# Optimization experiments

Measured on AMD Instinct MI355X. Metric: run time of the kernel, lower is better.

The kernel has to match this reference:

```python
import jax, jax.numpy as jnp
import numpy as np
from jax import lax

N, D, M, H = 8192, 32, 8, 128
ATOL = 1e-5
RTOL = 1e-5
MAX_STEPS = 10   # bounded adaptive dopri5 iterations (accept/reject with masking)
DT0 = 0.25


def setup_inputs() -> dict:
    key = jax.random.key(0)
    ks = jax.random.split(key, 6)
    p = lambda k, shape, s: jax.random.normal(k, shape, jnp.float32) * s
    return {
        "z": jax.random.normal(ks[0], (N, D), jnp.float32),
        "G_w": p(ks[1], (M, D), 0.3),
        "W1": p(ks[2], (H, D), (1.0 / D) ** 0.5),
        "b1": jnp.zeros((H,), jnp.float32),
        "W2": p(ks[3], (H, H), (1.0 / H) ** 0.5),
        "b2": jnp.zeros((H,), jnp.float32),
        "W3": p(ks[4], (D, H), (1.0 / H) ** 0.5),
        "b3": jnp.zeros((D,), jnp.float32),
        "T": jnp.ones((1,), jnp.float32),
    }


def qpnf_forward(z, G_w, W1, b1, W2, b2, W3, b3, T):
    d = z.shape[1]

    def mlp(x):  # dF network: d -> 128 -> 128 -> d
        h = jax.nn.relu(x @ W1.T + b1)
        h = jax.nn.relu(h @ W2.T + b2)
        return h @ W3.T + b3

    # G is linear (no bias) so jacrev(G)(x) == G_w for every sample; the batched
    # dG @ dG^T solves collapse to one shared (m,m) solve / (d,d) projector.
    A = G_w @ G_w.T                       # (m, m)
    AinvG = jnp.linalg.solve(A, G_w)      # (m, d) = A^{-1} W
    P = G_w.T @ AinvG                     # (d, d) null-space projector W^T A^{-1} W
    IP = jnp.eye(d, dtype=z.dtype) - P
    trP = jnp.trace(P)

    jac_mlp = jax.vmap(jax.jacrev(lambda xi: mlp(xi[None, :])[0]))  # (N,d,d)

    def f(y):  # augmented state y = [x | logp], dlogp/dt = -div(dx/dx)
        x = y[:, :d]
        dF = mlp(x)                        # (N, d)
        g = x @ G_w.T                      # (N, m)
        dz = -(dF @ IP) - g @ AinvG        # -(eta_J) - (eta_C)
        JdF = jac_mlp(x)                   # (N, d, d)
        # J_f = -(I-P) JdF - P  ->  dlogp = -trace(J_f)
        dlogp = jnp.einsum('jk,nkj->n', IP, JdF) + trP
        return jnp.concatenate([dz, dlogp[:, None]], axis=1)

    def rk_step(y, dt):  # Dormand-Prince 5(4)
        k1 = f(y)
        k2 = f(y + dt * (0.2 * k1))
        k3 = f(y + dt * (3/40 * k1 + 9/40 * k2))
        k4 = f(y + dt * (44/45 * k1 - 56/15 * k2 + 32/9 * k3))
        k5 = f(y + dt * (19372/6561 * k1 - 25360/2187 * k2 + 64448/6561 * k3 - 212/729 * k4))
        k6 = f(y + dt * (9017/3168 * k1 - 355/33 * k2 + 46732/5247 * k3 + 49/176 * k4 - 5103/18656 * k5))
        y1 = y + dt * (35/384 * k1 + 500/1113 * k3 + 125/192 * k4 - 2187/6784 * k5 + 11/84 * k6)
        k7 = f(y1)
        err = dt * ((35/384 - 5179/57600) * k1 + (500/1113 - 7571/16695) * k3
                    + (125/192 - 393/640) * k4 + (-2187/6784 + 92097/339200) * k5
                    + (11/84 - 187/2100) * k6 - (1/40) * k7)
        return y1, err

    t1 = 2.0 * T[0]  # eval path: integration_times[-1] *= 2
    y0 = jnp.concatenate([z, jnp.zeros((z.shape[0], 1), z.dtype)], axis=1)

    def body(carry, _):
        t, dt, y = carry
        done = t >= t1 - 1e-9
        dtc = jnp.where(done, jnp.asarray(1e-3, z.dtype), jnp.minimum(dt, t1 - t))
        y1, ev = rk_step(y, dtc)
        tol = ATOL + RTOL * jnp.maximum(jnp.abs(y), jnp.abs(y1))
        errn = jnp.sqrt(jnp.mean((ev / tol) ** 2))
        accept = jnp.logical_and(~done, errn <= 1.0)
        y_new = jnp.where(accept, y1, y)
        t_new = jnp.where(accept, t + dtc, t)
        factor = jnp.clip(0.9 * errn ** (-0.2), 0.2, 10.0)
        dt_new = jnp.where(done, dt, jnp.clip(dtc * factor, 1e-6, t1))
        dt_new = lax.stop_gradient(dt_new)
        return (t_new, dt_new, y_new), None

    init = (jnp.asarray(0.0, z.dtype), jnp.asarray(DT0, z.dtype), y0)
    (_, _, yT), _ = lax.scan(body, init, None, length=MAX_STEPS)
    return yT[:, :d]


def reference(z, G_w, W1, b1, W2, b2, W3, b3, T):
    return qpnf_forward(z, G_w, W1, b1, W2, b2, W3, b3, T)
```

## Files before the change

kernel.cpp:

```cpp
#include <hip/hip_runtime.h>
#include <hip/hip_cooperative_groups.h>
#include <math.h>

namespace cg = cooperative_groups;
typedef float4 f4;

#define NT 512
#define RB 32

#define WS_WR    0
#define WS_PART  32768
#define WS_TOTAL 35328

#define L_W1T   0
#define L_C3T   4096
#define L_P     8320
#define L_PT    9344
#define L_HST   10496
#define L_HS2   15104
#define L_XST   19712
#define L_B1    20864
#define L_B2    20992
#define L_C0    21120
#define L_GS    21152
#define L_AAUG  21408
#define L_AINVG 21536
#define L_MISC  21792
#define L_KZ    21796
#define L_KL    29860
#define L_YZ    30084
#define L_Y1Z   31236
#define L_YL    32388
#define L_Y1L   32420
#define LDS_FLOATS 32452
#define L_RED   L_XST

__device__ const float ACO[5][5] = {
  { 0.2f, 0.f, 0.f, 0.f, 0.f },
  { (float)(3.0/40.0), (float)(9.0/40.0), 0.f, 0.f, 0.f },
  { (float)(44.0/45.0), (float)(-56.0/15.0), (float)(32.0/9.0), 0.f, 0.f },
  { (float)(19372.0/6561.0), (float)(-25360.0/2187.0), (float)(64448.0/6561.0), (float)(-212.0/729.0), 0.f },
  { (float)(9017.0/3168.0), (float)(-355.0/33.0), (float)(46732.0/5247.0), (float)(49.0/176.0), (float)(-5103.0/18656.0) }
};

#define B1C ((float)(35.0/384.0))
#define B3C ((float)(500.0/1113.0))
#define B4C ((float)(125.0/192.0))
#define B5C ((float)(-2187.0/6784.0))
#define B6C ((float)(11.0/84.0))

#define E1C ((float)(35.0/384.0 - 5179.0/57600.0))
#define E3C ((float)(500.0/1113.0 - 7571.0/16695.0))
#define E4C ((float)(125.0/192.0 - 393.0/640.0))
#define E5C ((float)(-2187.0/6784.0 + 92097.0/339200.0))
#define E6C ((float)(11.0/84.0 - 187.0/2100.0))
#define E7C ((float)(-1.0/40.0))

__device__ __forceinline__ f4 ld4(const float* p){ return *(const f4*)p; }
__device__ __forceinline__ void st4(float* p, f4 v){ *(f4*)p = v; }

__device__ void assemble_x(float* lds, int tid, float dtc, const float* co, int np)
{
  __syncthreads();
  if (tid < 256){
    const int r = tid >> 3, jj = (tid & 7) * 4;
    const int o = r * 36 + jj;
    f4 y = ld4(&lds[L_YZ + o]);
    float sx = 0.f, sy = 0.f, sz = 0.f, sw = 0.f;
    for (int p = 0; p < np; p++){
      f4 kv = ld4(&lds[L_KZ + p * 1152 + o]);
      float c = co[p];
      sx += c * kv.x; sy += c * kv.y; sz += c * kv.z; sw += c * kv.w;
    }
    lds[L_XST + (jj + 0) * 36 + r] = y.x + dtc * sx;
    lds[L_XST + (jj + 1) * 36 + r] = y.y + dtc * sy;
    lds[L_XST + (jj + 2) * 36 + r] = y.z + dtc * sz;
    lds[L_XST + (jj + 3) * 36 + r] = y.w + dtc * sw;
  }
  __syncthreads();
}

__device__ void eval_f(float* lds, const float* __restrict__ ws, int tid,
                       float trP, int kout)
{
  const int cg = tid & 31, kh = (tid >> 5) & 1, wv = tid >> 6;
  const int row4 = 4 * wv;

  float a1[4][4];
#pragma unroll
  for (int i = 0; i < 4; i++)
#pragma unroll
    for (int j = 0; j < 4; j++) a1[i][j] = 0.f;
#pragma unroll 4
  for (int t = 0; t < 16; t++){
    const int k = kh * 16 + t;
    f4 av = ld4(&lds[L_XST + k * 36 + row4]);
    f4 bv = ld4(&lds[L_W1T + k * 128 + 4 * cg]);
    const float* ap = (const float*)&av;
    const float* bp = (const float*)&bv;
#pragma unroll
    for (int i = 0; i < 4; i++)
#pragma unroll
      for (int j = 0; j < 4; j++) a1[i][j] += bp[i] * ap[j];
  }
#pragma unroll
  for (int i = 0; i < 4; i++)
#pragma unroll
    for (int j = 0; j < 4; j++) a1[i][j] += __shfl_xor(a1[i][j], 32);
  if (kh == 0){
    f4 b1v = ld4(&lds[L_B1 + 4 * cg]);
    const float* b1p = (const float*)&b1v;
#pragma unroll
    for (int i = 0; i < 4; i++){
      f4 hv; float* hp = (float*)&hv;
#pragma unroll
      for (int j = 0; j < 4; j++) hp[j] = fmaxf(a1[i][j] + b1p[i], 0.f);
      st4(&lds[L_HST + (4 * cg + i) * 36 + row4], hv);
    }
  }
  __syncthreads();

  float ah[4][4], at[4][4];
#pragma unroll
  for (int i = 0; i < 4; i++)
#pragma unroll
    for (int j = 0; j < 4; j++){ ah[i][j] = 0.f; at[i][j] = 0.f; }
  const f4* WR4 = (const f4*)&ws[WS_WR];
  const int kb = kh * 64;
  f4 wb[4], rb[4];
#pragma unroll
  for (int u = 0; u < 4; u++){
    wb[u] = WR4[(kb + u) * 64 + cg];
    rb[u] = WR4[(kb + u) * 64 + 32 + cg];
  }
#pragma unroll 1
  for (int g = 0; g < 16; g++){
    f4 wc[4], rc[4];
#pragma unroll
    for (int u = 0; u < 4; u++){ wc[u] = wb[u]; rc[u] = rb[u]; }
    if (g < 15){
      const int kn = kb + (g + 1) * 4;
#pragma unroll
      for (int u = 0; u < 4; u++){
        wb[u] = WR4[(kn + u) * 64 + cg];
        rb[u] = WR4[(kn + u) * 64 + 32 + cg];
      }
    }
#pragma unroll
    for (int u = 0; u < 4; u++){
      const int k = kb + g * 4 + u;
      f4 av = ld4(&lds[L_HST + k * 36 + row4]);
      const float* ap = (const float*)&av;
      const float* wp = (const float*)&wc[u];
      const float* rp = (const float*)&rc[u];
      float m[4];
#pragma unroll
      for (int j = 0; j < 4; j++) m[j] = (ap[j] > 0.f) ? 1.f : 0.f;
#pragma unroll
      for (int i = 0; i < 4; i++)
#pragma unroll
        for (int j = 0; j < 4; j++){
          ah[i][j] += wp[i] * ap[j];
          at[i][j] += rp[i] * m[j];
        }
    }
  }
#pragma unroll
  for (int i = 0; i < 4; i++)
#pragma unroll
    for (int j = 0; j < 4; j++){
      ah[i][j] += __shfl_xor(ah[i][j], 32);
      at[i][j] += __shfl_xor(at[i][j], 32);
    }

  f4 b2v = ld4(&lds[L_B2 + 4 * cg]);
  const float* b2p = (const float*)&b2v;
  float h2v[4][4]; float dl[4] = {0.f, 0.f, 0.f, 0.f};
#pragma unroll
  for (int i = 0; i < 4; i++)
#pragma unroll
    for (int j = 0; j < 4; j++){
      float pre = ah[i][j] + b2p[i];
      float hv = fmaxf(pre, 0.f);
      h2v[i][j] = hv;
      if (pre > 0.f) dl[j] += at[i][j];
    }
#pragma unroll
  for (int mk = 1; mk < 32; mk <<= 1){
#pragma unroll
    for (int j = 0; j < 4; j++) dl[j] += __shfl_xor(dl[j], mk, 64);
  }
  if (kh == 0){
#pragma unroll
    for (int i = 0; i < 4; i++){
      f4 hv; float* hp = (float*)&hv;
#pragma unroll
      for (int j = 0; j < 4; j++) hp[j] = h2v[i][j];
      st4(&lds[L_HS2 + (4 * cg + i) * 36 + row4], hv);
    }
    if (cg == 0){
#pragma unroll
      for (int j = 0; j < 4; j++)
        lds[L_KL + kout * 32 + row4 + j] = dl[j] + trP;
    }
  }
  __syncthreads();

  float a3[4] = {0.f, 0.f, 0.f, 0.f};
  const int bb = kh * 64;
#pragma unroll 4
  for (int t = 0; t < 16; t++){
    f4 cv = ld4(&lds[L_C3T + cg * 132 + bb + 4 * t]);
    const float* cp = (const float*)&cv;
#pragma unroll
    for (int u = 0; u < 4; u++){
      f4 av = ld4(&lds[L_HS2 + (bb + 4 * t + u) * 36 + row4]);
      const float* ap = (const float*)&av;
#pragma unroll
      for (int j = 0; j < 4; j++) a3[j] += ap[j] * cp[u];
    }
  }
  const int qq = kh * 16;
#pragma unroll
  for (int t = 0; t < 4; t++){
    f4 pv = ld4(&lds[L_PT + cg * 36 + qq + 4 * t]);
    const float* pp = (const float*)&pv;
#pragma unroll
    for (int u = 0; u < 4; u++){
      f4 av = ld4(&lds[L_XST + (qq + 4 * t + u) * 36 + row4]);
      const float* ap = (const float*)&av;
#pragma unroll
      for (int j = 0; j < 4; j++) a3[j] += ap[j] * pp[u];
    }
  }
#pragma unroll
  for (int j = 0; j < 4; j++) a3[j] += __shfl_xor(a3[j], 32);
  if (kh == 0){
    float c0v = lds[L_C0 + cg];
#pragma unroll
    for (int j = 0; j < 4; j++)
      lds[L_KZ + kout * 1152 + (row4 + j) * 36 + cg] = -(a3[j] + c0v);
  }
}

__global__ void __launch_bounds__(NT, 2)
qpnf_kernel(const float* __restrict__ z, const float* __restrict__ Gw,
            const float* __restrict__ W1g, const float* __restrict__ b1g,
            const float* __restrict__ W2g, const float* __restrict__ b2g,
            const float* __restrict__ W3g, const float* __restrict__ b3g,
            const float* __restrict__ Tg, float* __restrict__ out,
            float* __restrict__ ws)
{
  __shared__ float lds[LDS_FLOATS];
  const int tid = threadIdx.x;
  const int bid = blockIdx.x;
  const int r0 = bid * RB;
  cg::grid_group grid = cg::this_grid();

  for (int i = 0; i < 8; i++){
    int idx = tid + i * NT;
    int h = idx >> 5, j = idx & 31;
    lds[L_W1T + j * 128 + h] = W1g[idx];
  }
  if (tid < 128){ lds[L_B1 + tid] = b1g[tid]; lds[L_B2 + tid] = b2g[tid]; }
  if (tid < 256) lds[L_GS + tid] = Gw[tid];
  __syncthreads();

  if (tid < 64){
    int i = tid >> 3, j = tid & 7;
    float s = 0.f;
    for (int k = 0; k < 32; k++) s += lds[L_GS + i * 32 + k] * lds[L_GS + j * 32 + k];
    lds[L_AAUG + i * 16 + j] = s;
    lds[L_AAUG + i * 16 + 8 + j] = (i == j) ? 1.f : 0.f;
  }
  __syncthreads();
  if (tid == 0){
    float* A = &lds[L_AAUG];
    for (int c = 0; c < 8; c++){
      int p = c; float mx = fabsf(A[c * 16 + c]);
      for (int r = c + 1; r < 8; r++){
        float v = fabsf(A[r * 16 + c]);
        if (v > mx){ mx = v; p = r; }
      }
      if (p != c)
        for (int q = 0; q < 16; q++){ float t = A[c*16+q]; A[c*16+q] = A[p*16+q]; A[p*16+q] = t; }
      float pv = 1.0f / A[c * 16 + c];
      for (int q = 0; q < 16; q++) A[c * 16 + q] *= pv;
      for (int r = 0; r < 8; r++) if (r != c){
        float fct = A[r * 16 + c];
        for (int q = 0; q < 16; q++) A[r * 16 + q] -= fct * A[c * 16 + q];
      }
    }
  }
  __syncthreads();
  if (tid < 256){
    int m = tid >> 5, d = tid & 31;
    float s = 0.f;
    for (int q = 0; q < 8; q++) s += lds[L_AAUG + m * 16 + 8 + q] * lds[L_GS + q * 32 + d];
    lds[L_AINVG + m * 32 + d] = s;
  }
  __syncthreads();
  for (int i4 = 0; i4 < 2; i4++){
    int idx = tid + i4 * NT;
    int i = idx >> 5, j = idx & 31;
    float s = 0.f;
    for (int m = 0; m < 8; m++) s += lds[L_GS + m * 32 + i] * lds[L_AINVG + m * 32 + j];
    lds[L_P + i * 32 + j] = s;
  }
  __syncthreads();
  float* IPl = &lds[L_XST];
  for (int i4 = 0; i4 < 2; i4++){
    int idx = tid + i4 * NT;
    int i = idx >> 5, j = idx & 31;
    IPl[i * 32 + j] = ((i == j) ? 1.f : 0.f) - lds[L_P + i * 32 + j];
  }
  if (tid == 0){
    float s = 0.f;
    for (int i = 0; i < 32; i++) s += lds[L_P + i * 32 + i];
    lds[L_MISC] = s;
  }
  __syncthreads();
  for (int i4 = 0; i4 < 8; i4++){
    int idx = tid + i4 * NT;
    int b = idx & 127, c = idx >> 7;
    float s = 0.f;
    for (int i = 0; i < 32; i++) s += W3g[i * 128 + b] * IPl[i * 32 + c];
    lds[L_C3T + c * 132 + b] = s;
  }
  for (int i4 = 0; i4 < 2; i4++){
    int idx = tid + i4 * NT;
    int c = idx >> 5, q = idx & 31;
    lds[L_PT + c * 36 + q] = lds[L_P + q * 32 + c];
  }
  if (tid < 32){
    float s = 0.f;
    for (int i = 0; i < 32; i++) s += b3g[i] * IPl[i * 32 + tid];
    lds[L_C0 + tid] = s;
  }
  for (int i4 = 0; i4 < 8; i4++){
    int idx = tid + i4 * NT;
    int j = idx >> 7, b = idx & 127;
    float s = 0.f;
    for (int k = 0; k < 32; k++) s += IPl[j * 32 + k] * W3g[k * 128 + b];
    lds[L_HST + j * 128 + b] = s;
  }
  __syncthreads();
  if (bid < 128 && tid < 128){
    int a = bid;
    float s = 0.f;
    for (int j = 0; j < 32; j++) s += W1g[a * 32 + j] * lds[L_HST + j * 128 + tid];
    ws[WS_WR + a * 256 + 128 + tid] = s * W2g[tid * 128 + a];
  }
  if (bid >= 128 && tid < 128){
    int a = bid - 128;
    ws[WS_WR + a * 256 + tid] = W2g[tid * 128 + a];
  }
  if (tid < 256){
    const int r = tid >> 3, jj = (tid & 7) * 4;
    st4(&lds[L_YZ + r * 36 + jj], ld4(&z[(r0 + r) * 32 + jj]));
  }
  if (tid < RB) lds[L_YL + tid] = 0.f;

  const float trP = lds[L_MISC];
  const float t1 = 2.0f * Tg[0];

  grid.sync();

  float t_cur = 0.f, dt_cur = 0.25f;
  bool prev_acc = false;

  for (int step = 0; step < 10; step++){
    if (t_cur >= t1 - 1e-9f) break;
    const float dtc = fminf(dt_cur, t1 - t_cur);

    for (int s = 1; s <= 6; s++){
      if (s == 1 && step > 0){
        if (prev_acc){
          if (tid < 256){
            const int r = tid >> 3, jj = (tid & 7) * 4;
            const int o = r * 36 + jj;
            st4(&lds[L_KZ + o], ld4(&lds[L_KZ + 6 * 1152 + o]));
          }
          if (tid < RB) lds[L_KL + tid] = lds[L_KL + 6 * 32 + tid];
        }
        continue;
      }
      assemble_x(lds, tid, dtc, ACO[s >= 2 ? s - 2 : 0], s - 1);
      eval_f(lds, ws, tid, trP, s - 1);
    }

    __syncthreads();
    if (tid < 256){
      const int r = tid >> 3, jj = (tid & 7) * 4;
      const int o = r * 36 + jj;
      f4 y   = ld4(&lds[L_YZ + o]);
      f4 k1v = ld4(&lds[L_KZ + 0 * 1152 + o]);
      f4 k3v = ld4(&lds[L_KZ + 2 * 1152 + o]);
      f4 k4v = ld4(&lds[L_KZ + 3 * 1152 + o]);
      f4 k5v = ld4(&lds[L_KZ + 4 * 1152 + o]);
      f4 k6v = ld4(&lds[L_KZ + 5 * 1152 + o]);
      f4 x;
      x.x = y.x + dtc * (B1C*k1v.x + B3C*k3v.x + B4C*k4v.x + B5C*k5v.x + B6C*k6v.x);
      x.y = y.y + dtc * (B1C*k1v.y + B3C*k3v.y + B4C*k4v.y + B5C*k5v.y + B6C*k6v.y);
      x.z = y.z + dtc * (B1C*k1v.z + B3C*k3v.z + B4C*k4v.z + B5C*k5v.z + B6C*k6v.z);
      x.w = y.w + dtc * (B1C*k1v.w + B3C*k3v.w + B4C*k4v.w + B5C*k5v.w + B6C*k6v.w);
      st4(&lds[L_Y1Z + o], x);
      lds[L_XST + (jj + 0) * 36 + r] = x.x;
      lds[L_XST + (jj + 1) * 36 + r] = x.y;
      lds[L_XST + (jj + 2) * 36 + r] = x.z;
      lds[L_XST + (jj + 3) * 36 + r] = x.w;
    }
    if (tid < RB){
      float s = B1C * lds[L_KL + 0*32 + tid] + B3C * lds[L_KL + 2*32 + tid]
              + B4C * lds[L_KL + 3*32 + tid] + B5C * lds[L_KL + 4*32 + tid]
              + B6C * lds[L_KL + 5*32 + tid];
      lds[L_Y1L + tid] = lds[L_YL + tid] + dtc * s;
    }
    __syncthreads();
    eval_f(lds, ws, tid, trP, 6);
    __syncthreads();

    float sacc = 0.f;
    if (tid < 256){
      const int r = tid >> 3, jj = (tid & 7) * 4;
      const int o = r * 36 + jj;
      f4 k1v = ld4(&lds[L_KZ + 0 * 1152 + o]);
      f4 k3v = ld4(&lds[L_KZ + 2 * 1152 + o]);
      f4 k4v = ld4(&lds[L_KZ + 3 * 1152 + o]);
      f4 k5v = ld4(&lds[L_KZ + 4 * 1152 + o]);
      f4 k6v = ld4(&lds[L_KZ + 5 * 1152 + o]);
      f4 k7v = ld4(&lds[L_KZ + 6 * 1152 + o]);
      f4 yv  = ld4(&lds[L_YZ + o]);
      f4 y1v = ld4(&lds[L_Y1Z + o]);
      float ev, tol, q;
      ev = dtc * (E1C*k1v.x + E3C*k3v.x + E4C*k4v.x + E5C*k5v.x + E6C*k6v.x + E7C*k7v.x);
      tol = 1e-5f + 1e-5f * fmaxf(fabsf(yv.x), fabsf(y1v.x)); q = ev / tol; sacc += q * q;
      ev = dtc * (E1C*k1v.y + E3C*k3v.y + E4C*k4v.y + E5C*k5v.y + E6C*k6v.y + E7C*k7v.y);
      tol = 1e-5f + 1e-5f * fmaxf(fabsf(yv.y), fabsf(y1v.y)); q = ev / tol; sacc += q * q;
      ev = dtc * (E1C*k1v.z + E3C*k3v.z + E4C*k4v.z + E5C*k5v.z + E6C*k6v.z + E7C*k7v.z);
      tol = 1e-5f + 1e-5f * fmaxf(fabsf(yv.z), fabsf(y1v.z)); q = ev / tol; sacc += q * q;
      ev = dtc * (E1C*k1v.w + E3C*k3v.w + E4C*k4v.w + E5C*k5v.w + E6C*k6v.w + E7C*k7v.w);
      tol = 1e-5f + 1e-5f * fmaxf(fabsf(yv.w), fabsf(y1v.w)); q = ev / tol; sacc += q * q;
    }
    if (tid < RB){
      float evl = dtc * (E1C * lds[L_KL + 0*32 + tid] + E3C * lds[L_KL + 2*32 + tid]
                + E4C * lds[L_KL + 3*32 + tid] + E5C * lds[L_KL + 4*32 + tid]
                + E6C * lds[L_KL + 5*32 + tid] + E7C * lds[L_KL + 6*32 + tid]);
      float toll = 1e-5f + 1e-5f * fmaxf(fabsf(lds[L_YL + tid]), fabsf(lds[L_Y1L + tid]));
      float ql = evl / toll; sacc += ql * ql;
    }
    __syncthreads();
    lds[L_RED + tid] = sacc; __syncthreads();
    for (int o = 256; o > 0; o >>= 1){
      if (tid < o) lds[L_RED + tid] += lds[L_RED + tid + o];
      __syncthreads();
    }
    if (tid == 0) ws[WS_PART + step * 256 + bid] = lds[L_RED + 0];

    grid.sync();

    if (tid < 256) lds[L_RED + tid] = ws[WS_PART + step * 256 + tid];
    __syncthreads();
    for (int o = 128; o > 0; o >>= 1){
      if (tid < o) lds[L_RED + tid] += lds[L_RED + tid + o];
      __syncthreads();
    }
    const float errn = sqrtf(lds[L_RED + 0] / 270336.0f);
    __syncthreads();

    const bool accept = (errn <= 1.0f);
    if (accept){
      if (tid < 256){
        const int r = tid >> 3, jj = (tid & 7) * 4;
        const int o = r * 36 + jj;
        st4(&lds[L_YZ + o], ld4(&lds[L_Y1Z + o]));
      }
      if (tid < RB) lds[L_YL + tid] = lds[L_Y1L + tid];
      t_cur += dtc;
    }
    float fac = 0.9f * powf(errn, -0.2f);
    fac = fminf(fmaxf(fac, 0.2f), 10.0f);
    dt_cur = fminf(fmaxf(dtc * fac, 1e-6f), t1);
    prev_acc = accept;
  }

  __syncthreads();
  if (tid < 256){
    const int r = tid >> 3, jj = (tid & 7) * 4;
    st4(&out[(r0 + r) * 32 + jj], ld4(&lds[L_YZ + r * 36 + jj]));
  }
}

extern "C" void kernel_launch(void* const* d_in, const int* in_sizes, int n_in,
                              void* d_out, int out_size, void* d_ws, size_t ws_size,
                              hipStream_t stream)
{
  (void)in_sizes; (void)n_in; (void)out_size;
  const float* z  = (const float*)d_in[0];
  const float* Gw = (const float*)d_in[1];
  const float* W1 = (const float*)d_in[2];
  const float* b1 = (const float*)d_in[3];
  const float* W2 = (const float*)d_in[4];
  const float* b2 = (const float*)d_in[5];
  const float* W3 = (const float*)d_in[6];
  const float* b3 = (const float*)d_in[7];
  const float* T  = (const float*)d_in[8];
  float* out = (float*)d_out;
  float* ws  = (float*)d_ws;
  if (ws_size < (size_t)WS_TOTAL * sizeof(float)) return;

  void* args[] = { (void*)&z, (void*)&Gw, (void*)&W1, (void*)&b1, (void*)&W2,
                   (void*)&b2, (void*)&W3, (void*)&b3, (void*)&T, (void*)&out,
                   (void*)&ws };
  hipLaunchCooperativeKernel((const void*)qpnf_kernel, dim3(256), dim3(NT),
                             args, 0, stream);
}
```

Baseline: 1.302 ms.

## Give each wavefront private LDS tiles to drop block-wide barriers in stage evaluation

Reorganizes the LDS layout so each 64-lane wavefront owns its own 4-row slices of the input, hidden-layer-1 and hidden-layer-2 buffers. Stage assembly, state copy and the k7-to-k1 reuse are redistributed so each wavefront only touches its own rows, which lets several __syncthreads calls be removed. The block reductions for the error norm now use wavefront shuffles instead of a barrier-heavy tree in LDS. The cost is a tighter reliance on the wave-local ownership invariants, and LDS regions are aliased during setup.

```diff
diff --git a/kernel.cpp b/kernel.cpp
--- a/kernel.cpp
+++ b/kernel.cpp
@@ -4,6 +4,7 @@
 
 namespace cg = cooperative_groups;
 typedef float4 f4;
+typedef float2 f2;
 
 #define NT 512
 #define RB 32
@@ -14,26 +15,28 @@
 
 #define L_W1T   0
 #define L_C3T   4096
-#define L_P     8320
-#define L_PT    9344
-#define L_HST   10496
-#define L_HS2   15104
-#define L_XST   19712
-#define L_B1    20864
-#define L_B2    20992
-#define L_C0    21120
-#define L_GS    21152
-#define L_AAUG  21408
-#define L_AINVG 21536
-#define L_MISC  21792
-#define L_KZ    21796
-#define L_KL    29860
-#define L_YZ    30084
-#define L_Y1Z   31236
-#define L_YL    32388
-#define L_Y1L   32420
-#define LDS_FLOATS 32452
-#define L_RED   L_XST
+#define L_PT    8320
+#define L_XW    9472
+#define L_H1W   10496
+#define L_H2W   14592
+#define L_KZ    18688
+#define L_KL    26752
+#define L_YZ    26976
+#define L_Y1Z   28128
+#define L_YL    29280
+#define L_Y1L   29312
+#define L_B1    29344
+#define L_B2    29472
+#define L_C0    29600
+#define L_GS    29632
+#define L_AAUG  29888
+#define L_AINVG 30016
+#define L_MISC  30272
+#define LDS_FLOATS 30276
+#define L_RED   L_H1W
+#define L_P     L_H2W
+#define L_IP    (L_H2W + 1024)
+#define L_IPW3  L_KZ
 
 __device__ const float ACO[5][5] = {
   { 0.2f, 0.f, 0.f, 0.f, 0.f },
@@ -59,32 +62,32 @@
 __device__ __forceinline__ f4 ld4(const float* p){ return *(const f4*)p; }
 __device__ __forceinline__ void st4(float* p, f4 v){ *(f4*)p = v; }
 
-__device__ void assemble_x(float* lds, int tid, float dtc, const float* co, int np)
+__device__ __forceinline__ void assemble_x(float* lds, int tid, float dtc,
+                                           const float* co, int np)
 {
-  __syncthreads();
-  if (tid < 256){
-    const int r = tid >> 3, jj = (tid & 7) * 4;
-    const int o = r * 36 + jj;
-    f4 y = ld4(&lds[L_YZ + o]);
-    float sx = 0.f, sy = 0.f, sz = 0.f, sw = 0.f;
-    for (int p = 0; p < np; p++){
-      f4 kv = ld4(&lds[L_KZ + p * 1152 + o]);
-      float c = co[p];
-      sx += c * kv.x; sy += c * kv.y; sz += c * kv.z; sw += c * kv.w;
-    }
-    lds[L_XST + (jj + 0) * 36 + r] = y.x + dtc * sx;
-    lds[L_XST + (jj + 1) * 36 + r] = y.y + dtc * sy;
-    lds[L_XST + (jj + 2) * 36 + r] = y.z + dtc * sz;
-    lds[L_XST + (jj + 3) * 36 + r] = y.w + dtc * sw;
-  }
-  __syncthreads();
+  const int w = tid >> 6, lane = tid & 63;
+  const int r = lane >> 4;
+  const int c = (lane << 1) & 31;
+  const int o = (4 * w + r) * 36 + c;
+  f2 y = *(const f2*)&lds[L_YZ + o];
+  float sx = 0.f, sy = 0.f;
+  for (int p = 0; p < np; p++){
+    f2 kv = *(const f2*)&lds[L_KZ + p * 1152 + o];
+    sx += co[p] * kv.x; sy += co[p] * kv.y;
+  }
+  float* XWp = &lds[L_XW + w * 128];
+  XWp[(c + 0) * 4 + r] = y.x + dtc * sx;
+  XWp[(c + 1) * 4 + r] = y.y + dtc * sy;
 }
 
 __device__ void eval_f(float* lds, const float* __restrict__ ws, int tid,
                        float trP, int kout)
 {
-  const int cg = tid & 31, kh = (tid >> 5) & 1, wv = tid >> 6;
-  const int row4 = 4 * wv;
+  const int w = tid >> 6, lane = tid & 63;
+  const int cg = lane & 31, kh = lane >> 5;
+  float* XWp = &lds[L_XW  + w * 128];
+  float* H1p = &lds[L_H1W + w * 512];
+  float* H2p = &lds[L_H2W + w * 512];
 
   float a1[4][4];
 #pragma unroll
@@ -94,10 +97,10 @@
 #pragma unroll 4
   for (int t = 0; t < 16; t++){
     const int k = kh * 16 + t;
-    f4 av = ld4(&lds[L_XST + k * 36 + row4]);
-    f4 bv = ld4(&lds[L_W1T + k * 128 + 4 * cg]);
-    const float* ap = (const float*)&av;
-    const float* bp = (const float*)&bv;
+    f4 xv = ld4(&XWp[k * 4]);
+    f4 wv = ld4(&lds[L_W1T + k * 128 + 4 * cg]);
+    const float* ap = (const float*)&xv;
+    const float* bp = (const float*)&wv;
 #pragma unroll
     for (int i = 0; i < 4; i++)
 #pragma unroll
@@ -115,7 +118,7 @@
       f4 hv; float* hp = (float*)&hv;
 #pragma unroll
       for (int j = 0; j < 4; j++) hp[j] = fmaxf(a1[i][j] + b1p[i], 0.f);
-      st4(&lds[L_HST + (4 * cg + i) * 36 + row4], hv);
+      st4(&H1p[(4 * cg + i) * 4], hv);
     }
   }
   __syncthreads();
@@ -149,7 +152,7 @@
 #pragma unroll
     for (int u = 0; u < 4; u++){
       const int k = kb + g * 4 + u;
-      f4 av = ld4(&lds[L_HST + k * 36 + row4]);
+      f4 av = ld4(&H1p[k * 4]);
       const float* ap = (const float*)&av;
       const float* wp = (const float*)&wc[u];
       const float* rp = (const float*)&rc[u];
@@ -196,15 +199,14 @@
       f4 hv; float* hp = (float*)&hv;
 #pragma unroll
       for (int j = 0; j < 4; j++) hp[j] = h2v[i][j];
-      st4(&lds[L_HS2 + (4 * cg + i) * 36 + row4], hv);
+      st4(&H2p[(4 * cg + i) * 4], hv);
     }
     if (cg == 0){
 #pragma unroll
       for (int j = 0; j < 4; j++)
-        lds[L_KL + kout * 32 + row4 + j] = dl[j] + trP;
-    }
-  }
-  __syncthreads();
+        lds[L_KL + kout * 32 + 4 * w + j] = dl[j] + trP;
+    }
+  }
 
   float a3[4] = {0.f, 0.f, 0.f, 0.f};
   const int bb = kh * 64;
@@ -214,7 +216,7 @@
     const float* cp = (const float*)&cv;
 #pragma unroll
     for (int u = 0; u < 4; u++){
-      f4 av = ld4(&lds[L_HS2 + (bb + 4 * t + u) * 36 + row4]);
+      f4 av = ld4(&H2p[(bb + 4 * t + u) * 4]);
       const float* ap = (const float*)&av;
 #pragma unroll
       for (int j = 0; j < 4; j++) a3[j] += ap[j] * cp[u];
@@ -227,7 +229,7 @@
     const float* pp = (const float*)&pv;
 #pragma unroll
     for (int u = 0; u < 4; u++){
-      f4 av = ld4(&lds[L_XST + (qq + 4 * t + u) * 36 + row4]);
+      f4 av = ld4(&XWp[(qq + 4 * t + u) * 4]);
       const float* ap = (const float*)&av;
 #pragma unroll
       for (int j = 0; j < 4; j++) a3[j] += ap[j] * pp[u];
@@ -239,7 +241,7 @@
     float c0v = lds[L_C0 + cg];
 #pragma unroll
     for (int j = 0; j < 4; j++)
-      lds[L_KZ + kout * 1152 + (row4 + j) * 36 + cg] = -(a3[j] + c0v);
+      lds[L_KZ + kout * 1152 + (4 * w + j) * 36 + cg] = -(a3[j] + c0v);
   }
 }
 
@@ -308,7 +310,7 @@
     lds[L_P + i * 32 + j] = s;
   }
   __syncthreads();
-  float* IPl = &lds[L_XST];
+  float* IPl = &lds[L_IP];
   for (int i4 = 0; i4 < 2; i4++){
     int idx = tid + i4 * NT;
     int i = idx >> 5, j = idx & 31;
@@ -342,13 +344,13 @@
     int j = idx >> 7, b = idx & 127;
     float s = 0.f;
     for (int k = 0; k < 32; k++) s += IPl[j * 32 + k] * W3g[k * 128 + b];
-    lds[L_HST + j * 128 + b] = s;
+    lds[L_IPW3 + j * 128 + b] = s;
   }
   __syncthreads();
   if (bid < 128 && tid < 128){
     int a = bid;
     float s = 0.f;
-    for (int j = 0; j < 32; j++) s += W1g[a * 32 + j] * lds[L_HST + j * 128 + tid];
+    for (int j = 0; j < 32; j++) s += W1g[a * 32 + j] * lds[L_IPW3 + j * 128 + tid];
     ws[WS_WR + a * 256 + 128 + tid] = s * W2g[tid * 128 + a];
   }
   if (bid >= 128 && tid < 128){
@@ -376,12 +378,11 @@
     for (int s = 1; s <= 6; s++){
       if (s == 1 && step > 0){
         if (prev_acc){
-          if (tid < 256){
-            const int r = tid >> 3, jj = (tid & 7) * 4;
-            const int o = r * 36 + jj;
-            st4(&lds[L_KZ + o], ld4(&lds[L_KZ + 6 * 1152 + o]));
-          }
-          if (tid < RB) lds[L_KL + tid] = lds[L_KL + 6 * 32 + tid];
+          const int w = tid >> 6, lane = tid & 63;
+          const int r = lane >> 4, c = (lane << 1) & 31;
+          const int o = (4 * w + r) * 36 + c;
+          *(f2*)&lds[L_KZ + o] = *(const f2*)&lds[L_KZ + 6 * 1152 + o];
+          if (lane < 4) lds[L_KL + 4 * w + lane] = lds[L_KL + 6 * 32 + 4 * w + lane];
         }
         continue;
       }
@@ -405,10 +406,12 @@
       x.z = y.z + dtc * (B1C*k1v.z + B3C*k3v.z + B4C*k4v.z + B5C*k5v.z + B6C*k6v.z);
       x.w = y.w + dtc * (B1C*k1v.w + B3C*k3v.w + B4C*k4v.w + B5C*k5v.w + B6C*k6v.w);
       st4(&lds[L_Y1Z + o], x);
-      lds[L_XST + (jj + 0) * 36 + r] = x.x;
-      lds[L_XST + (jj + 1) * 36 + r] = x.y;
-      lds[L_XST + (jj + 2) * 36 + r] = x.z;
-      lds[L_XST + (jj + 3) * 36 + r] = x.w;
+      float* XWp = &lds[L_XW + (r >> 2) * 128];
+      const int rr = r & 3;
+      XWp[(jj + 0) * 4 + rr] = x.x;
+      XWp[(jj + 1) * 4 + rr] = x.y;
+      XWp[(jj + 2) * 4 + rr] = x.z;
+      XWp[(jj + 3) * 4 + rr] = x.w;
     }
     if (tid < RB){
       float s = B1C * lds[L_KL + 0*32 + tid] + B3C * lds[L_KL + 2*32 + tid]
@@ -449,33 +452,35 @@
       float toll = 1e-5f + 1e-5f * fmaxf(fabsf(lds[L_YL + tid]), fabsf(lds[L_Y1L + tid]));
       float ql = evl / toll; sacc += ql * ql;
     }
+#pragma unroll
+    for (int mk = 1; mk < 64; mk <<= 1) sacc += __shfl_xor(sacc, mk, 64);
+    if ((tid & 63) == 0) lds[L_RED + (tid >> 6)] = sacc;
     __syncthreads();
-    lds[L_RED + tid] = sacc; __syncthreads();
-    for (int o = 256; o > 0; o >>= 1){
-      if (tid < o) lds[L_RED + tid] += lds[L_RED + tid + o];
-      __syncthreads();
-    }
-    if (tid == 0) ws[WS_PART + step * 256 + bid] = lds[L_RED + 0];
+    if (tid == 0){
+      float s = lds[L_RED+0] + lds[L_RED+1] + lds[L_RED+2] + lds[L_RED+3]
+              + lds[L_RED+4] + lds[L_RED+5] + lds[L_RED+6] + lds[L_RED+7];
+      ws[WS_PART + step * 256 + bid] = s;
+    }
 
     grid.sync();
 
-    if (tid < 256) lds[L_RED + tid] = ws[WS_PART + step * 256 + tid];
+    float ps = 0.f;
+    if (tid < 256) ps = ws[WS_PART + step * 256 + tid];
+#pragma unroll
+    for (int mk = 1; mk < 64; mk <<= 1) ps += __shfl_xor(ps, mk, 64);
+    if (tid < 256 && (tid & 63) == 0) lds[L_RED + (tid >> 6)] = ps;
     __syncthreads();
-    for (int o = 128; o > 0; o >>= 1){
-      if (tid < o) lds[L_RED + tid] += lds[L_RED + tid + o];
-      __syncthreads();
-    }
-    const float errn = sqrtf(lds[L_RED + 0] / 270336.0f);
+    const float errn = sqrtf((lds[L_RED+0] + lds[L_RED+1] + lds[L_RED+2] + lds[L_RED+3])
+                             / 270336.0f);
     __syncthreads();
 
     const bool accept = (errn <= 1.0f);
     if (accept){
-      if (tid < 256){
-        const int r = tid >> 3, jj = (tid & 7) * 4;
-        const int o = r * 36 + jj;
-        st4(&lds[L_YZ + o], ld4(&lds[L_Y1Z + o]));
-      }
-      if (tid < RB) lds[L_YL + tid] = lds[L_Y1L + tid];
+      const int w = tid >> 6, lane = tid & 63;
+      const int r = lane >> 4, c = (lane << 1) & 31;
+      const int o = (4 * w + r) * 36 + c;
+      *(f2*)&lds[L_YZ + o] = *(const f2*)&lds[L_Y1Z + o];
+      if (lane < 4) lds[L_YL + 4 * w + lane] = lds[L_Y1L + 4 * w + lane];
       t_cur += dtc;
     }
     float fac = 0.9f * powf(errn, -0.2f);
```

New measurement: 1.189 ms. 8.7% less time.
